# Performance work log

Hardware: AMD Instinct MI355X
Metric: run time of the kernel (lower is better)

## Reference

```python
import jax, jax.numpy as jnp
import numpy as np

NUM_GROUPS = 8
EPS = 1e-5


def group_norm(x, scale, bias):
    # x: [b, c, h, w]; 8 groups, affine, eps=1e-5 (torch GroupNorm defaults)
    b, c, h, w = x.shape
    xg = x.reshape(b, NUM_GROUPS, c // NUM_GROUPS * h * w)
    mean = jnp.mean(xg, axis=-1, keepdims=True)
    var = jnp.var(xg, axis=-1, keepdims=True)
    xg = (xg - mean) * jax.lax.rsqrt(var + EPS)
    x = xg.reshape(b, c, h, w)
    return x * scale[None, :, None, None] + bias[None, :, None, None]


def conv1x1(x, w, bias):
    # 1x1 conv == per-pixel linear: x [b,c,h,w], w [c_out,c_in], bias [c_out]
    return jnp.einsum('oc,bchw->bohw', w, x) + bias[None, :, None, None]


def setup_inputs() -> dict:
    key = jax.random.key(0)
    ks = jax.random.split(key, 11)
    b, c, h, w = 8, 512, 32, 32
    init = 1.0 / np.sqrt(c)
    d = {
        'x': jax.random.normal(ks[0], (b, c, h, w), dtype=jnp.float32),
        'gn_scale': jnp.ones((c,), jnp.float32),
        'gn_bias': jnp.zeros((c,), jnp.float32),
        'wq': jax.random.uniform(ks[1], (c, c), jnp.float32, -init, init),
        'bq': jax.random.uniform(ks[2], (c,), jnp.float32, -init, init),
        'wk': jax.random.uniform(ks[3], (c, c), jnp.float32, -init, init),
        'bk': jax.random.uniform(ks[4], (c,), jnp.float32, -init, init),
        'wv': jax.random.uniform(ks[5], (c, c), jnp.float32, -init, init),
        'bv': jax.random.uniform(ks[6], (c,), jnp.float32, -init, init),
        'wproj': jax.random.uniform(ks[7], (c, c), jnp.float32, -init, init),
        'bproj': jax.random.uniform(ks[8], (c,), jnp.float32, -init, init),
    }
    return d


def reference(x, gn_scale, gn_bias, wq, bq, wk, bk, wv, bv, wproj, bproj):
    b, c, h, w = x.shape
    h_ = group_norm(x, gn_scale, gn_bias)
    q = conv1x1(h_, wq, bq).reshape(b, c, h * w)  # [b,c,hw]
    k = conv1x1(h_, wk, bk).reshape(b, c, h * w)
    v = conv1x1(h_, wv, bv).reshape(b, c, h * w)
    scale = 1.0 / np.sqrt(c).astype(np.float32)
    # scores[b,i,j] = sum_c q[b,c,i]*k[b,c,j]
    scores = jnp.einsum('bci,bcj->bij', q, k) * scale
    attn = jax.nn.softmax(scores, axis=2)  # softmax over j (keys)
    # h_[b,c,i] = sum_j v[b,c,j] * attn[b,i,j]
    out = jnp.einsum('bcj,bij->bci', v, attn).reshape(b, c, h, w)
    out = conv1x1(out, wproj, bproj)
    return x + out
```

## Files before the change

kernel.cpp:

```cpp
#include <hip/hip_runtime.h>
#include <hip/hip_bf16.h>

#define DI __device__ __forceinline__

typedef __bf16 bf16x8 __attribute__((ext_vector_type(8)));
typedef float f32x4 __attribute__((ext_vector_type(4)));

typedef const void __attribute__((address_space(1))) gas_t;
typedef void __attribute__((address_space(3))) las_t;

DI unsigned short f2bf(float f) {
    unsigned u = __builtin_bit_cast(unsigned, f);
    u += 0x7fffu + ((u >> 16) & 1u);
    return (unsigned short)(u >> 16);
}

template <int ROWS>
DI void stage_tile(const unsigned short* __restrict__ g, int ldK,
                   unsigned short* lds, int t) {
    int row_in = t >> 3;
    int kg = (t & 7) ^ (row_in & 7);
    const unsigned short* src = g + (size_t)row_in * ldK + kg * 8;
    unsigned short* dst = lds + ((t >> 6) << 9);
#pragma unroll
    for (int c = 0; c < ROWS / 32; ++c) {
        __builtin_amdgcn_global_load_lds(
            (gas_t*)(unsigned long long)(src + (size_t)c * 32 * ldK),
            (las_t*)(unsigned)(unsigned long long)(dst + c * 2048),
            16, 0, 0);
    }
}

DI bf16x8 frag(const unsigned short* lds, int r, int kg) {
    return *(const bf16x8*)((const char*)lds + r * 128 + ((kg ^ (r & 7)) << 4));
}

template <int MR>
DI void compute_step(const unsigned short* As_, const unsigned short* Bs_,
                     f32x4 (&acc)[MR][4], int wm, int wn, int l15, int lks) {
#pragma unroll
    for (int kk = 0; kk < 2; ++kk) {
        bf16x8 a_[MR], b_[4];
#pragma unroll
        for (int m = 0; m < MR; ++m) a_[m] = frag(As_, wm + m * 16 + l15, kk * 4 + lks);
#pragma unroll
        for (int n = 0; n < 4; ++n) b_[n] = frag(Bs_, wn + n * 16 + l15, kk * 4 + lks);
#pragma unroll
        for (int m = 0; m < MR; ++m)
#pragma unroll
            for (int n = 0; n < 4; ++n)
                acc[m][n] = __builtin_amdgcn_mfma_f32_16x16x32_bf16(a_[m], b_[n], acc[m][n], 0, 0, 0);
    }
}

template <int TM, int MODE, int PIPE>
DI void gemm_phase(unsigned short* AsB, unsigned short* BsB,
                   const unsigned short* __restrict__ A, const unsigned short* __restrict__ B,
                   const float* __restrict__ b0, const float* __restrict__ b1,
                   const float* __restrict__ b2,
                   void* __restrict__ C0, void* __restrict__ C1, void* __restrict__ C2,
                   const float* __restrict__ resid, float* __restrict__ spart,
                   int M, int N, int K, float scale, size_t sA, size_t sB, size_t sC,
                   int bx, int t) {
    constexpr int MR = TM / 32;
    constexpr int ABUF = TM * 64;
    constexpr int BBUF = 128 * 64;
    int b = bx & 7;
    int tile = bx >> 3;
    int nTx = N >> 7;
    int tx = tile % nTx, ty = tile / nTx;
    int m0 = ty * TM, n0 = tx << 7;
    const unsigned short* Ag = A + sA * b + (size_t)m0 * K;
    const unsigned short* Bg = B + sB * b + (size_t)n0 * K;
    int lane = t & 63, wid = t >> 6;
    int wm = (wid >> 1) * (TM / 2), wn = (wid & 1) * 64;
    const int l15 = lane & 15, lks = lane >> 4;
    const int rbase = lks * 4;

    f32x4 acc[MR][4];
#pragma unroll
    for (int i = 0; i < MR; ++i)
#pragma unroll
        for (int j = 0; j < 4; ++j) acc[i][j] = (f32x4){0.f, 0.f, 0.f, 0.f};

    float inv[4];
    if constexpr (MODE == 2) {
#pragma unroll
        for (int n = 0; n < 4; ++n) {
            int ng = n0 + wn + n * 16 + l15;
            float ssum = 0.f;
#pragma unroll
            for (int k = 0; k < 16; ++k) ssum += spart[(size_t)(b * 16 + k) * 1024 + ng];
            inv[n] = 1.f / ssum;
        }
    }
    float bn4[4];
    if constexpr (MODE == 3) {
#pragma unroll
        for (int n = 0; n < 4; ++n) bn4[n] = b0[n0 + wn + n * 16 + l15];
    }

    if constexpr (PIPE == 0) {
        for (int k0 = 0; k0 < K; k0 += 64) {
            stage_tile<TM>(Ag + k0, K, AsB, t);
            stage_tile<128>(Bg + k0, K, BsB, t);
            asm volatile("s_waitcnt vmcnt(0)" ::: "memory");
            __syncthreads();
            compute_step<MR>(AsB, BsB, acc, wm, wn, l15, lks);
            __syncthreads();
        }
    } else {
        stage_tile<TM>(Ag, K, AsB, t);
        stage_tile<128>(Bg, K, BsB, t);
        asm volatile("s_waitcnt vmcnt(0)" ::: "memory");
        __syncthreads();
        int cur = 0;
        for (int k0 = 0; k0 < K; k0 += 64) {
            if (k0 + 64 < K) {
                stage_tile<TM>(Ag + k0 + 64, K, AsB + (cur ^ 1) * ABUF, t);
                stage_tile<128>(Bg + k0 + 64, K, BsB + (cur ^ 1) * BBUF, t);
            }
            compute_step<MR>(AsB + cur * ABUF, BsB + cur * BBUF, acc, wm, wn, l15, lks);
            if (k0 + 64 < K) {
                asm volatile("s_waitcnt vmcnt(0)" ::: "memory");
                __syncthreads();
            }
            cur ^= 1;
        }
    }

    const size_t cb = sC * b;
    if constexpr (MODE == 0) {
#pragma unroll
        for (int m = 0; m < MR; ++m) {
            int mgg = m0 + wm + m * 16 + rbase;
            int region = mgg >> 9;
            int local = mgg & 511;
            const float* bias = (region == 0) ? b0 : (region == 1) ? b1 : b2;
            float bv4[4];
#pragma unroll
            for (int j = 0; j < 4; ++j) bv4[j] = bias[local + j];
            if (region < 2) {
                unsigned short* Ct = (unsigned short*)(region == 0 ? C0 : C1) + cb;
#pragma unroll
                for (int n = 0; n < 4; ++n) {
                    int ng = n0 + wn + n * 16 + l15;
                    f32x4 v = acc[m][n];
                    ushort4 o;
                    o.x = f2bf(v[0] + bv4[0]); o.y = f2bf(v[1] + bv4[1]);
                    o.z = f2bf(v[2] + bv4[2]); o.w = f2bf(v[3] + bv4[3]);
                    *(ushort4*)&Ct[(size_t)ng * 512 + local] = o;
                }
            } else {
                unsigned short* Vb = (unsigned short*)C2 + cb;
#pragma unroll
                for (int n = 0; n < 4; ++n) {
                    int ng = n0 + wn + n * 16 + l15;
                    f32x4 v = acc[m][n];
#pragma unroll
                    for (int j = 0; j < 4; ++j)
                        Vb[(size_t)(local + j) * 1024 + ng] = f2bf(v[j] + bv4[j]);
                }
            }
        }
    } else if constexpr (MODE == 1) {
        unsigned short* Ct = (unsigned short*)C0 + cb;
        float psum[4] = {0.f, 0.f, 0.f, 0.f};
#pragma unroll
        for (int m = 0; m < MR; ++m) {
            int mg = m0 + wm + m * 16 + rbase;
#pragma unroll
            for (int n = 0; n < 4; ++n) {
                int ng = n0 + wn + n * 16 + l15;
                f32x4 v = acc[m][n];
                float e0 = __expf(v[0] * scale), e1 = __expf(v[1] * scale);
                float e2 = __expf(v[2] * scale), e3 = __expf(v[3] * scale);
                psum[n] += (e0 + e1) + (e2 + e3);
                ushort4 o;
                o.x = f2bf(e0); o.y = f2bf(e1); o.z = f2bf(e2); o.w = f2bf(e3);
                *(ushort4*)&Ct[(size_t)ng * M + mg] = o;
            }
        }
        int rb = (m0 >> 7) * 2 + (wid >> 1);
#pragma unroll
        for (int n = 0; n < 4; ++n) {
            float p = psum[n];
            p += __shfl_xor(p, 16);
            p += __shfl_xor(p, 32);
            if (lks == 0) {
                int ng = n0 + wn + n * 16 + l15;
                spart[(size_t)(b * 16 + rb) * 1024 + ng] = p;
            }
        }
    } else if constexpr (MODE == 2) {
        unsigned short* Ct = (unsigned short*)C0 + cb;
#pragma unroll
        for (int m = 0; m < MR; ++m) {
            int mg = m0 + wm + m * 16 + rbase;
#pragma unroll
            for (int n = 0; n < 4; ++n) {
                int ng = n0 + wn + n * 16 + l15;
                f32x4 v = acc[m][n];
                ushort4 o;
                o.x = f2bf(v[0] * inv[n]); o.y = f2bf(v[1] * inv[n]);
                o.z = f2bf(v[2] * inv[n]); o.w = f2bf(v[3] * inv[n]);
                *(ushort4*)&Ct[(size_t)ng * M + mg] = o;
            }
        }
    } else {
        float* Cf = (float*)C0 + cb;
#pragma unroll
        for (int m = 0; m < MR; ++m) {
            int mg = m0 + wm + m * 16 + rbase;
#pragma unroll
            for (int n = 0; n < 4; ++n) {
                int ng = n0 + wn + n * 16 + l15;
                f32x4 v = acc[m][n];
                const float* rp = resid + cb + (size_t)ng * M + mg;
                float4 o;
                o.x = v[0] + bn4[n] + rp[0]; o.y = v[1] + bn4[n] + rp[1];
                o.z = v[2] + bn4[n] + rp[2]; o.w = v[3] + bn4[n] + rp[3];
                *(float4*)&Cf[(size_t)ng * M + mg] = o;
            }
        }
    }
}

DI void stats_body(const float* __restrict__ x, float2* __restrict__ part,
                   float* red, int bx, int t) {
    int b = bx & 7, g = (bx >> 3) & 7, ch = bx >> 6;
    size_t base = ((size_t)b * 512 + g * 64 + ch * 8) * 1024;
    const float4* xp = (const float4*)(x + base);
    float s = 0.f, q = 0.f;
#pragma unroll
    for (int it = 0; it < 8; ++it) {
        float4 v = xp[it * 256 + t];
        s += (v.x + v.y) + (v.z + v.w);
        q += (v.x * v.x + v.y * v.y) + (v.z * v.z + v.w * v.w);
    }
#pragma unroll
    for (int o = 32; o; o >>= 1) { s += __shfl_xor(s, o); q += __shfl_xor(q, o); }
    int lane = t & 63, wid = t >> 6;
    if (!lane) { red[wid] = s; red[4 + wid] = q; }
    __syncthreads();
    if (t == 0)
        part[((b * 8 + g) * 8) + ch] =
            make_float2(red[0] + red[1] + red[2] + red[3],
                        red[4] + red[5] + red[6] + red[7]);
}

__global__ __launch_bounds__(256) void prep_kernel(const float* __restrict__ x,
                                                   float2* __restrict__ part,
                                                   const float* __restrict__ w0,
                                                   const float* __restrict__ w1,
                                                   const float* __restrict__ w2,
                                                   const float* __restrict__ w3,
                                                   unsigned short* __restrict__ wb) {
    __shared__ float red[8];
    int bx = blockIdx.x, t = threadIdx.x;
    if (bx < 512) {
        stats_body(x, part, red, bx, t);
    } else {
        int chunk = bx - 512;
        int w = chunk >> 8;
        const float* sp = (w == 0) ? w0 : (w == 1) ? w1 : (w == 2) ? w2 : w3;
        unsigned short* o = wb + (size_t)w * 262144;
        int idx = (chunk & 255) * 256 + t;
        float4 v = ((const float4*)sp)[idx];
        ushort4 r;
        r.x = f2bf(v.x); r.y = f2bf(v.y); r.z = f2bf(v.z); r.w = f2bf(v.w);
        ((ushort4*)o)[idx] = r;
    }
}

__global__ __launch_bounds__(256) void gn_applyT(const float* __restrict__ x,
                                                 const float2* __restrict__ part,
                                                 const float* __restrict__ gs,
                                                 const float* __restrict__ gb,
                                                 unsigned short* __restrict__ hT) {
    __shared__ unsigned short tile[128 * 66];
    int bx = blockIdx.x, t = threadIdx.x;
    int b = bx & 7, g = (bx >> 3) & 7, ic = bx >> 6;
    int bg = b * 8 + g;
    float s = 0.f, q = 0.f;
#pragma unroll
    for (int k = 0; k < 8; ++k) { float2 p = part[bg * 8 + k]; s += p.x; q += p.y; }
    float mean = s * (1.f / 65536.f);
    float var = q * (1.f / 65536.f) - mean * mean;
    float rstd = rsqrtf(var + 1e-5f);

    int i4 = t & 31, cq = t >> 5;
    size_t xbase = ((size_t)b * 512 + g * 64) * 1024 + ic * 128;
#pragma unroll
    for (int pass = 0; pass < 8; ++pass) {
        int c = pass * 8 + cq;
        float4 v = *(const float4*)&x[xbase + (size_t)c * 1024 + i4 * 4];
        int gc = g * 64 + c;
        float sc = gs[gc] * rstd, bi = gb[gc] - mean * sc;
        unsigned short* tp = &tile[(i4 * 4) * 66 + c];
        tp[0]   = f2bf(v.x * sc + bi);
        tp[66]  = f2bf(v.y * sc + bi);
        tp[132] = f2bf(v.z * sc + bi);
        tp[198] = f2bf(v.w * sc + bi);
    }
    __syncthreads();
    int i = t >> 1, h = t & 1;
    const unsigned short* tp2 = &tile[i * 66 + h * 32];
    unsigned short* op = &hT[(size_t)b * (1024 * 512) + (size_t)(ic * 128 + i) * 512 + g * 64 + h * 32];
#pragma unroll
    for (int cc = 0; cc < 4; ++cc) {
        unsigned short tmp[8];
#pragma unroll
        for (int j = 0; j < 8; ++j) tmp[j] = tp2[cc * 8 + j];
        *(uint4*)&op[cc * 8] = *(const uint4*)tmp;
    }
}

template <int TM, int MODE, int MINW, int PIPE>
__global__ __launch_bounds__(256, MINW) void gemm_bt(
        const unsigned short* __restrict__ A, const unsigned short* __restrict__ B,
        const float* __restrict__ b0, const float* __restrict__ b1,
        const float* __restrict__ b2,
        void* __restrict__ C0, void* __restrict__ C1, void* __restrict__ C2,
        const float* __restrict__ resid, float* __restrict__ spart,
        int M, int N, int K, float scale, size_t sA, size_t sB, size_t sC) {
    constexpr int NBUF = PIPE ? 2 : 1;
    __shared__ __align__(16) unsigned short As[NBUF * TM * 64];
    __shared__ __align__(16) unsigned short Bs[NBUF * 128 * 64];
    gemm_phase<TM, MODE, PIPE>(As, Bs, A, B, b0, b1, b2, C0, C1, C2, resid, spart,
                               M, N, K, scale, sA, sB, sC, blockIdx.x, threadIdx.x);
}

extern "C" void kernel_launch(void* const* d_in, const int* in_sizes, int n_in,
                              void* d_out, int out_size, void* d_ws, size_t ws_size,
                              hipStream_t stream) {
    const float* x  = (const float*)d_in[0];
    const float* gs = (const float*)d_in[1];
    const float* gb = (const float*)d_in[2];
    const float* wq = (const float*)d_in[3];
    const float* bq = (const float*)d_in[4];
    const float* wk = (const float*)d_in[5];
    const float* bk = (const float*)d_in[6];
    const float* wv = (const float*)d_in[7];
    const float* bv = (const float*)d_in[8];
    const float* wp = (const float*)d_in[9];
    const float* bp = (const float*)d_in[10];
    float* out = (float*)d_out;

    char* ws = (char*)d_ws;
    const size_t MB = 1u << 20;
    unsigned short* hT = (unsigned short*)(ws + 0);
    unsigned short* wb = (unsigned short*)(ws + 8 * MB);
    unsigned short* qT = (unsigned short*)(ws + 10 * MB);
    unsigned short* kT = (unsigned short*)(ws + 18 * MB);
    unsigned short* vN = (unsigned short*)(ws + 26 * MB);
    unsigned short* E  = (unsigned short*)(ws + 34 * MB);
    unsigned short* OT = (unsigned short*)(ws + 50 * MB);
    float2* gnpart     = (float2*)(ws + 58 * MB);
    float*  spart      = (float*)(ws + 58 * MB + 65536);

    const unsigned short* wpb = wb + 3 * 262144;
    const size_t sH = 1024 * 512;
    const size_t sS = 1024 * 1024;

    prep_kernel<<<1536, 256, 0, stream>>>(x, gnpart, wq, wk, wv, wp, wb);
    gn_applyT<<<512, 256, 0, stream>>>(x, gnpart, gs, gb, hT);

    gemm_bt<192, 0, 2, 1><<<512, 256, 0, stream>>>(
        wb, hT, bq, bk, bv, qT, kT, vN, nullptr, nullptr,
        1536, 1024, 512, 1.f, 0, sH, sH);
    gemm_bt<128, 1, 2, 1><<<512, 256, 0, stream>>>(
        kT, qT, nullptr, nullptr, nullptr, E, nullptr, nullptr, nullptr, spart,
        1024, 1024, 512, 0.044194173824159216f, sH, sH, sS);
    gemm_bt<64, 2, 2, 1><<<512, 256, 0, stream>>>(
        vN, E, nullptr, nullptr, nullptr, OT, nullptr, nullptr, nullptr, spart,
        512, 1024, 1024, 1.f, sH, sS, sH);
    gemm_bt<64, 3, 2, 1><<<512, 256, 0, stream>>>(
        OT, wpb, bp, nullptr, nullptr, out, nullptr, nullptr, x, nullptr,
        1024, 512, 512, 1.f, sH, 0, sH);
}
```

Measured before the change: 77.25 us.

## Swap QK operand order so softmax rows map to M and retile QKV GEMM

The scores GEMM now takes q as the M operand and k as the N operand. The epilogue writes E row-major with scalar bf16 stores and reduces the row sums across the 16 lanes of each row with shuffles. The partial-sum index changes from m-block to n-block/wave. The QKV projection GEMM moves from a 192-row tile to a 128-row tile with 768 blocks and different template flags, which raises parallelism. The scalar strided stores in the scores epilogue may lose coalescing compared with the previous ushort4 stores, and correctness depends on the PV kernel's reading of E and spart matching the new layout.

```diff
diff --git a/kernel.cpp b/kernel.cpp
--- a/kernel.cpp
+++ b/kernel.cpp
@@ -164,32 +164,32 @@
             }
         }
     } else if constexpr (MODE == 1) {
-        unsigned short* Ct = (unsigned short*)C0 + cb;
-        float psum[4] = {0.f, 0.f, 0.f, 0.f};
+        unsigned short* Eb = (unsigned short*)C0 + cb;
+        int part = tx * 2 + (wid & 1);
 #pragma unroll
         for (int m = 0; m < MR; ++m) {
-            int mg = m0 + wm + m * 16 + rbase;
+            float ps[4] = {0.f, 0.f, 0.f, 0.f};
 #pragma unroll
             for (int n = 0; n < 4; ++n) {
-                int ng = n0 + wn + n * 16 + l15;
+                int jg = n0 + wn + n * 16 + l15;
                 f32x4 v = acc[m][n];
-                float e0 = __expf(v[0] * scale), e1 = __expf(v[1] * scale);
-                float e2 = __expf(v[2] * scale), e3 = __expf(v[3] * scale);
-                psum[n] += (e0 + e1) + (e2 + e3);
-                ushort4 o;
-                o.x = f2bf(e0); o.y = f2bf(e1); o.z = f2bf(e2); o.w = f2bf(e3);
-                *(ushort4*)&Ct[(size_t)ng * M + mg] = o;
-            }
-        }
-        int rb = (m0 >> 7) * 2 + (wid >> 1);
-#pragma unroll
-        for (int n = 0; n < 4; ++n) {
-            float p = psum[n];
-            p += __shfl_xor(p, 16);
-            p += __shfl_xor(p, 32);
-            if (lks == 0) {
-                int ng = n0 + wn + n * 16 + l15;
-                spart[(size_t)(b * 16 + rb) * 1024 + ng] = p;
+#pragma unroll
+                for (int jr = 0; jr < 4; ++jr) {
+                    float e = __expf(v[jr] * scale);
+                    ps[jr] += e;
+                    int row = m0 + wm + m * 16 + rbase + jr;
+                    Eb[(size_t)row * N + jg] = f2bf(e);
+                }
+            }
+#pragma unroll
+            for (int jr = 0; jr < 4; ++jr) {
+                float p = ps[jr];
+                p += __shfl_xor(p, 1); p += __shfl_xor(p, 2);
+                p += __shfl_xor(p, 4); p += __shfl_xor(p, 8);
+                if (l15 == 0) {
+                    int row = m0 + wm + m * 16 + rbase + jr;
+                    spart[(size_t)(b * 16 + part) * 1024 + row] = p;
+                }
             }
         }
     } else if constexpr (MODE == 2) {
@@ -366,11 +366,11 @@
     prep_kernel<<<1536, 256, 0, stream>>>(x, gnpart, wq, wk, wv, wp, wb);
     gn_applyT<<<512, 256, 0, stream>>>(x, gnpart, gs, gb, hT);
 
-    gemm_bt<192, 0, 2, 1><<<512, 256, 0, stream>>>(
+    gemm_bt<128, 0, 3, 0><<<768, 256, 0, stream>>>(
         wb, hT, bq, bk, bv, qT, kT, vN, nullptr, nullptr,
         1536, 1024, 512, 1.f, 0, sH, sH);
     gemm_bt<128, 1, 2, 1><<<512, 256, 0, stream>>>(
-        kT, qT, nullptr, nullptr, nullptr, E, nullptr, nullptr, nullptr, spart,
+        qT, kT, nullptr, nullptr, nullptr, E, nullptr, nullptr, nullptr, spart,
         1024, 1024, 512, 0.044194173824159216f, sH, sH, sS);
     gemm_bt<64, 2, 2, 1><<<512, 256, 0, stream>>>(
         vN, E, nullptr, nullptr, nullptr, OT, nullptr, nullptr, nullptr, spart,
```

After: 76.85 us. No clear change (-0.5%).
